# Performance work log

Hardware: AMD Instinct MI355X
Metric: run time of the kernel (lower is better)

## Reference

```python
import jax, jax.numpy as jnp
import numpy as np

DIM = 384
NH = 16
HD = DIM // NH          # 24
HID = DIM * 4           # titan/cms hidden
RD = 2 * (HD // 3 // 2) # 8 rope channels per axis (d/h/w), 3*RD == HD


def _ln(x, scale, bias):
    m = x.mean(-1, keepdims=True)
    v = ((x - m) ** 2).mean(-1, keepdims=True)
    return (x - m) * jax.lax.rsqrt(v + 1e-5) * scale + bias


def _mlp(x, w1, b1, w2, b2):
    # TitanMemory / CMS level: Linear -> GELU -> Linear (titan_layers=2)
    h = jax.nn.gelu(x @ w1 + b1, approximate=False)
    return h @ w2 + b2


def _rotate(x, pos):
    # rotate_queries_or_keys: interleaved rotary. x: [B,nh,N,d], pos: [N]
    d = x.shape[-1]
    inv_freq = 1.0 / (10000.0 ** (jnp.arange(0, d, 2, dtype=jnp.float32) / d))
    ang = pos[:, None] * inv_freq[None, :]              # [N, d/2]
    sin, cos = jnp.sin(ang), jnp.cos(ang)
    x1, x2 = x[..., 0::2], x[..., 1::2]
    y1 = x1 * cos - x2 * sin
    y2 = x1 * sin + x2 * cos
    return jnp.stack([y1, y2], axis=-1).reshape(x.shape)


def _rope3d(q, T, H, W):
    # 3D RoPE on frame tokens (action_tokens=0): time / height / width axes
    B, N, D = q.shape
    qh = q.reshape(B, N, NH, HD).transpose(0, 2, 1, 3)   # [B,nh,N,hd]
    ids = jnp.arange(T * H * W)
    tpos = (ids // (H * W)).astype(jnp.float32)
    hpos = ((ids % (H * W)) // W).astype(jnp.float32)
    wpos = (ids % W).astype(jnp.float32)
    qd = _rotate(qh[..., :RD], tpos)
    qhh = _rotate(qh[..., RD:2 * RD], hpos)
    qww = _rotate(qh[..., 2 * RD:3 * RD], wpos)
    out = jnp.concatenate([qd, qhh, qww], axis=-1)
    return out.transpose(0, 2, 1, 3).reshape(B, N, D)


def setup_inputs() -> dict:
    key = jax.random.key(0)
    ks = jax.random.split(key, 8)
    B, T, H, W = 8, 8, 16, 16
    N = T * H * W
    p = lambda k, sh: jax.random.normal(k, sh, jnp.float32) * 0.02
    return {
        "x": jax.random.normal(ks[0], (B, N, DIM), jnp.float32),
        "norm1_scale": jnp.ones((DIM,), jnp.float32),
        "norm1_bias": jnp.zeros((DIM,), jnp.float32),
        "norm2_scale": jnp.ones((DIM,), jnp.float32),
        "norm2_bias": jnp.zeros((DIM,), jnp.float32),
        "q_w": p(ks[1], (DIM, DIM)),
        # stacked Titan memories: [M_k, M_v, M_eta, M_alpha, M_memory]
        "titan_w1": p(ks[2], (5, DIM, HID)),
        "titan_b1": jnp.zeros((5, HID), jnp.float32),
        "titan_w2": p(ks[3], (5, HID, DIM)),
        "titan_b2": jnp.zeros((5, DIM), jnp.float32),
        "out_w": p(ks[4], (DIM, DIM)),
        "out_b": jnp.zeros((DIM,), jnp.float32),
        # CMS levels: [fast, medium, slow]
        "cms_w1": p(ks[5], (3, DIM, HID)),
        "cms_b1": jnp.zeros((3, HID), jnp.float32),
        "cms_w2": p(ks[6], (3, HID, DIM)),
        "cms_b2": jnp.zeros((3, DIM), jnp.float32),
        "T": T, "H": H, "W": W, "action_tokens": 0,
    }


def reference(x, norm1_scale, norm1_bias, norm2_scale, norm2_bias, q_w,
              titan_w1, titan_b1, titan_w2, titan_b2, out_w, out_b,
              cms_w1, cms_b1, cms_w2, cms_b2, T, H, W, action_tokens):
    # Phase A: self-modifying Titan (eval path: retrieval only)
    y = _ln(x, norm1_scale, norm1_bias)
    q = y @ q_w                                  # static query projection (Eq. 76)
    q = _rope3d(q, T, H, W)                      # 3D RoPE (action_tokens == 0)
    out = _mlp(q, titan_w1[4], titan_b1[4], titan_w2[4], titan_b2[4])  # M_memory(q)
    out = out @ out_w + out_b                    # out_proj
    x = x + out                                  # residual (drop_path = identity)
    # Phase B: CMS multi-frequency MLP cascade
    y = _ln(x, norm2_scale, norm2_bias)
    cms = sum(_mlp(y, cms_w1[i], cms_b1[i], cms_w2[i], cms_b2[i]) for i in range(3))
    return x + cms
```

## Files before the change

### kernel.cpp

```cpp
#include <hip/hip_runtime.h>
#include <math.h>

typedef unsigned short u16;
typedef unsigned int u32;
typedef __attribute__((ext_vector_type(8))) short short8;
typedef __attribute__((ext_vector_type(4))) float f32x4;

#define DIM 384
#define HID 1536

static __device__ __forceinline__ float bf2f(u32 b){ return __uint_as_float(b << 16); }
static __device__ __forceinline__ u16 f2bf(float f){
  u32 u = __float_as_uint(f);
  u32 r = (u + 0x7fffu + ((u >> 16) & 1u)) >> 16;
  return (u16)r;
}
static __device__ __forceinline__ float gelu_fast(float v){
  float u = v * fmaf(0.0713548162726f, v * v, 1.59576912161f);
  float e = exp2f(-1.44269504089f * u);
  return v * __builtin_amdgcn_rcpf(1.0f + e);
}
static __device__ __forceinline__ void gload_lds16(const u16* g, u16* l){
  __builtin_amdgcn_global_load_lds(
      (__attribute__((address_space(1))) void*)(void*)const_cast<u16*>(g),
      (__attribute__((address_space(3))) void*)(void*)l, 16, 0, 0);
}

__global__ __launch_bounds__(256) void ln_kernel(const float* __restrict__ x,
    const float* __restrict__ sc, const float* __restrict__ bi, u16* __restrict__ y){
  int lane = threadIdx.x & 63;
  int row = blockIdx.x * 4 + (threadIdx.x >> 6);
  const float* xr = x + (size_t)row * DIM;
  float v[6];
  float s = 0.f, sq = 0.f;
#pragma unroll
  for (int i = 0; i < 6; ++i){
    float f = xr[lane + 64*i];
    v[i] = f; s += f; sq += f*f;
  }
#pragma unroll
  for (int o = 1; o < 64; o <<= 1){ s += __shfl_xor(s, o); sq += __shfl_xor(sq, o); }
  float mean = s * (1.0f/DIM);
  float var = sq * (1.0f/DIM) - mean*mean;
  float inv = rsqrtf(var + 1e-5f);
  u16* yr = y + (size_t)row * DIM;
#pragma unroll
  for (int i = 0; i < 6; ++i){
    int c = lane + 64*i;
    yr[c] = f2bf((v[i] - mean) * inv * sc[c] + bi[c]);
  }
}

__global__ __launch_bounds__(256) void rope_kernel(u16* __restrict__ q,
    const int* __restrict__ Tp, const int* __restrict__ Hp, const int* __restrict__ Wp,
    int Mtok){
  int idx = blockIdx.x * 256 + threadIdx.x;
  int tok = idx / 192;
  if (tok >= Mtok) return;
  int p = idx - tok * 192;
  int H = *Hp, W = *Wp, T = *Tp;
  int HW = H * W;
  int Ns = T * HW;
  int n = tok % Ns;
  int head = p / 12;
  int pp = p - head * 12;
  int s = pp >> 2, f = pp & 3;
  float pos;
  if (s == 0)      pos = (float)(n / HW);
  else if (s == 1) pos = (float)((n / W) % H);
  else             pos = (float)(n % W);
  const float LOG2_10000 = 13.28771237954945f;
  float inv = exp2f(-0.25f * (float)f * LOG2_10000);
  float ang = pos * inv;
  float sn = sinf(ang), cs = cosf(ang);
  size_t base = (size_t)tok * DIM + head * 24 + s * 8 + 2 * f;
  u32 u = *(u32*)(q + base);
  float x1 = bf2f(u & 0xffffu), x2 = bf2f(u >> 16);
  float y1 = x1 * cs - x2 * sn;
  float y2 = x1 * sn + x2 * cs;
  *(u32*)(q + base) = (u32)f2bf(y1) | ((u32)f2bf(y2) << 16);
}

template<int R, int C>
__global__ __launch_bounds__(256) void transpose_kernel(
    const float* __restrict__ s0, const float* __restrict__ s1,
    const float* __restrict__ s2, const float* __restrict__ s3,
    u16* __restrict__ d0, u16* __restrict__ d1, u16* __restrict__ d2, u16* __restrict__ d3,
    int dstStride){
  const float* src = (blockIdx.z == 0) ? s0 : (blockIdx.z == 1) ? s1 : (blockIdx.z == 2) ? s2 : s3;
  u16* dst         = (blockIdx.z == 0) ? d0 : (blockIdx.z == 1) ? d1 : (blockIdx.z == 2) ? d2 : d3;
  __shared__ u16 t[32][33];
  int tx = threadIdx.x & 31, ty = threadIdx.x >> 5;
  int r0 = blockIdx.y * 32, c0 = blockIdx.x * 32;
#pragma unroll
  for (int i = 0; i < 4; ++i)
    t[ty + 8*i][tx] = f2bf(src[(size_t)(r0 + ty + 8*i) * C + c0 + tx]);
  __syncthreads();
#pragma unroll
  for (int i = 0; i < 4; ++i)
    dst[(size_t)(c0 + ty + 8*i) * dstStride + r0 + tx] = t[tx][ty + 8*i];
}

__global__ void bias3_kernel(const float* __restrict__ b, float* __restrict__ o){
  int n = threadIdx.x;
  o[n] = b[n] + b[384 + n] + b[768 + n];
}

enum { E_NONE = 0, E_BIAS = 1, E_BIAS_GELU = 2, E_RES_F32 = 3, E_ACC_F32 = 4, E_FINAL = 5 };

template<int BM, int N, int K, int EPI>
__global__ __launch_bounds__(256) void gemm_kernel(
    const u16* __restrict__ A, const u16* __restrict__ Bt,
    void* __restrict__ Cv, const float* __restrict__ bias,
    const float* __restrict__ res, float* __restrict__ accbuf){
  constexpr int BN = 128, BK = 64;
  constexpr int MT = BM / 32, NT = 4;
  constexpr int AIT = BM / 32, BIT = 4;
  __shared__ __align__(16) u16 As[BM * BK];
  __shared__ __align__(16) u16 Bs[BN * BK];
  const int tid = threadIdx.x;
  const int lane = tid & 63;
  const int wv = tid >> 6;
  const int wm = (wv >> 1) * (BM / 2);
  const int wn = (wv & 1) * 64;
  const int quad = lane >> 4;
  const int l16 = lane & 15;
  const int rsw = l16 & 7;
  const size_t m0 = (size_t)blockIdx.x * BM;
  const int n0 = blockIdx.y * BN;
  const int srow = lane >> 3;
  const int scol = ((lane & 7) ^ srow) * 8;

  f32x4 acc[MT][NT];
  const f32x4 zero = {0.f, 0.f, 0.f, 0.f};
#pragma unroll
  for (int mt = 0; mt < MT; ++mt)
#pragma unroll
    for (int nt = 0; nt < NT; ++nt) acc[mt][nt] = zero;

  for (int kt = 0; kt < K; kt += BK){
#pragma unroll
    for (int i = 0; i < AIT; ++i){
      int seg = i * 4 + wv;
      gload_lds16(A + (m0 + (size_t)(seg * 8 + srow)) * K + kt + scol, As + seg * 512);
    }
#pragma unroll
    for (int i = 0; i < BIT; ++i){
      int seg = i * 4 + wv;
      gload_lds16(Bt + (size_t)(n0 + seg * 8 + srow) * K + kt + scol, Bs + seg * 512);
    }
    __syncthreads();
#pragma unroll
    for (int kk = 0; kk < 2; ++kk){
      short8 af[MT], bfr[NT];
#pragma unroll
      for (int mt = 0; mt < MT; ++mt)
        af[mt] = *(const short8*)(As + (wm + mt*16 + l16) * BK + (((kk*4 + quad) ^ rsw) << 3));
#pragma unroll
      for (int nt = 0; nt < NT; ++nt)
        bfr[nt] = *(const short8*)(Bs + (wn + nt*16 + l16) * BK + (((kk*4 + quad) ^ rsw) << 3));
#pragma unroll
      for (int mt = 0; mt < MT; ++mt)
#pragma unroll
        for (int nt = 0; nt < NT; ++nt)
          acc[mt][nt] = __builtin_amdgcn_mfma_f32_16x16x32_bf16(af[mt], bfr[nt], acc[mt][nt], 0, 0, 0);
    }
    __syncthreads();
  }

#pragma unroll
  for (int mt = 0; mt < MT; ++mt){
#pragma unroll
    for (int nt = 0; nt < NT; ++nt){
      int ncol = n0 + wn + nt*16 + l16;
      float bv = (EPI != E_NONE) ? bias[ncol] : 0.f;
      size_t mbase = m0 + wm + mt*16 + quad*4;
#pragma unroll
      for (int r = 0; r < 4; ++r){
        size_t off = (mbase + r) * N + ncol;
        float vv = acc[mt][nt][r];
        if      (EPI == E_NONE)      ((u16*)Cv)[off] = f2bf(vv);
        else if (EPI == E_BIAS)      ((u16*)Cv)[off] = f2bf(vv + bv);
        else if (EPI == E_BIAS_GELU) ((u16*)Cv)[off] = f2bf(gelu_fast(vv + bv));
        else if (EPI == E_RES_F32)   accbuf[off] = vv + bv + res[off];
        else if (EPI == E_ACC_F32)   accbuf[off] += vv + bv;
        else            ((float*)Cv)[off] = accbuf[off] + vv + bv;
      }
    }
  }
}

template<int N, int K>
__global__ __launch_bounds__(256, 3) void gemm_up_kernel(
    const u16* __restrict__ A, const u16* __restrict__ Bt,
    u16* __restrict__ C, const float* __restrict__ bias){
  constexpr int BK = 64;
  __shared__ __align__(16) u16 As[64 * BK];
  __shared__ __align__(16) u16 Bs[256 * BK];
  const int tid = threadIdx.x;
  const int lane = tid & 63;
  const int wv = tid >> 6;
  const int wm = (wv >> 1) * 32;
  const int wn = (wv & 1) * 128;
  const int quad = lane >> 4;
  const int l16 = lane & 15;
  const int rsw = l16 & 7;
  const size_t m0 = (size_t)blockIdx.x * 64;
  const int n0 = blockIdx.y * 256;
  const int srow = lane >> 3;
  const int scol = ((lane & 7) ^ srow) * 8;

  f32x4 acc[2][8];
  const f32x4 zero = {0.f, 0.f, 0.f, 0.f};
#pragma unroll
  for (int mt = 0; mt < 2; ++mt)
#pragma unroll
    for (int nt = 0; nt < 8; ++nt) acc[mt][nt] = zero;

  for (int kt = 0; kt < K; kt += BK){
#pragma unroll
    for (int i = 0; i < 2; ++i){
      int seg = i * 4 + wv;
      gload_lds16(A + (m0 + (size_t)(seg * 8 + srow)) * K + kt + scol, As + seg * 512);
    }
#pragma unroll
    for (int i = 0; i < 8; ++i){
      int seg = i * 4 + wv;
      gload_lds16(Bt + (size_t)(n0 + seg * 8 + srow) * K + kt + scol, Bs + seg * 512);
    }
    __syncthreads();
#pragma unroll
    for (int kk = 0; kk < 2; ++kk){
      short8 af[2], bfr[8];
#pragma unroll
      for (int mt = 0; mt < 2; ++mt)
        af[mt] = *(const short8*)(As + (wm + mt*16 + l16) * BK + (((kk*4 + quad) ^ rsw) << 3));
#pragma unroll
      for (int nt = 0; nt < 8; ++nt)
        bfr[nt] = *(const short8*)(Bs + (wn + nt*16 + l16) * BK + (((kk*4 + quad) ^ rsw) << 3));
#pragma unroll
      for (int mt = 0; mt < 2; ++mt)
#pragma unroll
        for (int nt = 0; nt < 8; ++nt)
          acc[mt][nt] = __builtin_amdgcn_mfma_f32_16x16x32_bf16(af[mt], bfr[nt], acc[mt][nt], 0, 0, 0);
    }
    __syncthreads();
  }

#pragma unroll
  for (int mt = 0; mt < 2; ++mt){
#pragma unroll
    for (int nt = 0; nt < 8; ++nt){
      int ncol = n0 + wn + nt*16 + l16;
      float bv = bias[ncol];
      size_t mbase = m0 + wm + mt*16 + quad*4;
#pragma unroll
      for (int r = 0; r < 4; ++r)
        C[(mbase + r) * N + ncol] = f2bf(gelu_fast(acc[mt][nt][r] + bv));
    }
  }
}

extern "C" void kernel_launch(void* const* d_in, const int* in_sizes, int n_in,
                              void* d_out, int out_size, void* d_ws, size_t ws_size,
                              hipStream_t stream) {
  const int W11 = DIM * HID;
  const float* x   = (const float*)d_in[0];
  const float* n1s = (const float*)d_in[1];
  const float* n1b = (const float*)d_in[2];
  const float* n2s = (const float*)d_in[3];
  const float* n2b = (const float*)d_in[4];
  const float* qw  = (const float*)d_in[5];
  const float* tw1 = (const float*)d_in[6] + 4 * W11;
  const float* tb1 = (const float*)d_in[7] + 4 * HID;
  const float* tw2 = (const float*)d_in[8] + 4 * W11;
  const float* tb2 = (const float*)d_in[9] + 4 * DIM;
  const float* ow  = (const float*)d_in[10];
  const float* ob  = (const float*)d_in[11];
  const float* cw1 = (const float*)d_in[12];
  const float* cb1 = (const float*)d_in[13];
  const float* cw2 = (const float*)d_in[14];
  const float* cb2 = (const float*)d_in[15];
  const int* Tp = (const int*)d_in[16];
  const int* Hp = (const int*)d_in[17];
  const int* Wp = (const int*)d_in[18];
  const int M = in_sizes[0] / DIM;
  const bool fused = (ws_size >= 198772224u);

  char* ws = (char*)d_ws;
  u16 *y, *h, *qwT, *owT, *w1T, *w2T, *cw1T, *cw2T;
  float *x2, *cb2s = nullptr;
  u16* qb = (u16*)d_out;
  if (fused){
    y    = (u16*) (ws + 0);
    h    = (u16*) (ws + 12582912);
    x2   = (float*)(ws + 163577856);
    qwT  = (u16*) (ws + 188743680);
    owT  = (u16*) (ws + 189038592);
    w1T  = (u16*) (ws + 189333504);
    w2T  = (u16*) (ws + 190513152);
    cw1T = (u16*) (ws + 191692800);
    cw2T = (u16*) (ws + 195231744);
    cb2s = (float*)(ws + 198770688);
  } else {
    if (ws_size < 98107392u) return;
    y    = (u16*) (ws + 0);
    h    = (u16*) (ws + 12582912);
    x2   = (float*)(ws + 62914560);
    qwT  = (u16*) (ws + 88080384);
    owT  = (u16*) (ws + 88375296);
    w1T  = (u16*) (ws + 88670208);
    w2T  = (u16*) (ws + 89849856);
    cw1T = (u16*) (ws + 91029504);
    cw2T = (u16*) (ws + 94568448);
  }

  transpose_kernel<384,384><<<dim3(12,12,2),256,0,stream>>>(
      qw, ow, qw, qw, qwT, owT, qwT, qwT, 384);
  transpose_kernel<384,1536><<<dim3(48,12,4),256,0,stream>>>(
      tw1, cw1, cw1 + W11, cw1 + 2*W11, w1T, cw1T, cw1T + W11, cw1T + 2*W11, 384);
  if (fused){
    transpose_kernel<1536,384><<<dim3(12,48,1),256,0,stream>>>(
        tw2, tw2, tw2, tw2, w2T, w2T, w2T, w2T, 1536);
    transpose_kernel<1536,384><<<dim3(12,48,3),256,0,stream>>>(
        cw2, cw2 + W11, cw2 + 2*W11, cw2, cw2T, cw2T + 1536, cw2T + 3072, cw2T, 4608);
    bias3_kernel<<<1,384,0,stream>>>(cb2, cb2s);
  } else {
    transpose_kernel<1536,384><<<dim3(12,48,4),256,0,stream>>>(
        tw2, cw2, cw2 + W11, cw2 + 2*W11, w2T, cw2T, cw2T + W11, cw2T + 2*W11, 1536);
  }

  ln_kernel<<<M/4,256,0,stream>>>(x, n1s, n1b, y);
  gemm_kernel<64,384,384,E_NONE><<<dim3(M/64,3),256,0,stream>>>(y, qwT, qb, nullptr, nullptr, nullptr);
  rope_kernel<<<(M*192)/256,256,0,stream>>>(qb, Tp, Hp, Wp, M);
  gemm_up_kernel<1536,384><<<dim3(M/64,6),256,0,stream>>>(qb, w1T, h, tb1);
  gemm_kernel<64,384,1536,E_BIAS><<<dim3(M/64,3),256,0,stream>>>(h, w2T, qb, tb2, nullptr, nullptr);
  gemm_kernel<64,384,384,E_RES_F32><<<dim3(M/64,3),256,0,stream>>>(qb, owT, nullptr, ob, x, x2);
  ln_kernel<<<M/4,256,0,stream>>>(x2, n2s, n2b, y);
  if (fused){
    gemm_up_kernel<4608,384><<<dim3(M/64,18),256,0,stream>>>(y, cw1T, h, cb1);
    gemm_kernel<64,384,4608,E_FINAL><<<dim3(M/64,3),256,0,stream>>>(
        h, cw2T, d_out, cb2s, nullptr, x2);
  } else {
    for (int i = 0; i < 3; ++i){
      gemm_up_kernel<1536,384><<<dim3(M/64,6),256,0,stream>>>(y, cw1T + i*W11, h, cb1 + i*HID);
      if (i < 2)
        gemm_kernel<64,384,1536,E_ACC_F32><<<dim3(M/64,3),256,0,stream>>>(
            h, cw2T + i*W11, nullptr, cb2 + i*DIM, nullptr, x2);
      else
        gemm_kernel<64,384,1536,E_FINAL><<<dim3(M/64,3),256,0,stream>>>(
            h, cw2T + i*W11, d_out, cb2 + i*DIM, nullptr, x2);
    }
  }
}
```

Baseline: 400.1 us.

## Fuse MLP up and down projections, keeping GELU hidden chunks in LDS

```diff
diff --git a/kernel.cpp b/kernel.cpp
--- a/kernel.cpp
+++ b/kernel.cpp
@@ -17,7 +17,7 @@
 }
 static __device__ __forceinline__ float gelu_fast(float v){
   float u = v * fmaf(0.0713548162726f, v * v, 1.59576912161f);
-  float e = exp2f(-1.44269504089f * u);
+  float e = __builtin_amdgcn_exp2f(-1.44269504089f * u);
   return v * __builtin_amdgcn_rcpf(1.0f + e);
 }
 static __device__ __forceinline__ void gload_lds16(const u16* g, u16* l){
@@ -70,9 +70,9 @@
   else if (s == 1) pos = (float)((n / W) % H);
   else             pos = (float)(n % W);
   const float LOG2_10000 = 13.28771237954945f;
-  float inv = exp2f(-0.25f * (float)f * LOG2_10000);
+  float inv = __builtin_amdgcn_exp2f(-0.25f * (float)f * LOG2_10000);
   float ang = pos * inv;
-  float sn = sinf(ang), cs = cosf(ang);
+  float sn = __sinf(ang), cs = __cosf(ang);
   size_t base = (size_t)tok * DIM + head * 24 + s * 8 + 2 * f;
   u32 u = *(u32*)(q + base);
   float x1 = bf2f(u & 0xffffu), x2 = bf2f(u >> 16);
@@ -190,73 +190,139 @@
   }
 }
 
-template<int N, int K>
-__global__ __launch_bounds__(256, 3) void gemm_up_kernel(
-    const u16* __restrict__ A, const u16* __restrict__ Bt,
-    u16* __restrict__ C, const float* __restrict__ bias){
-  constexpr int BK = 64;
-  __shared__ __align__(16) u16 As[64 * BK];
-  __shared__ __align__(16) u16 Bs[256 * BK];
-  const int tid = threadIdx.x;
+template<int HIDT, int EPI>
+__global__ __launch_bounds__(512, 2) void fused_mlp_kernel(
+    const u16* __restrict__ A, const u16* __restrict__ W1t, const u16* __restrict__ W2t,
+    const float* __restrict__ b1, const float* __restrict__ b2,
+    float* __restrict__ accbuf, void* __restrict__ outp){
+  constexpr int BH = 256;
+  constexpr int NCH = HIDT / BH;
+  __shared__ __align__(16) u16 SB[(64 + BH) * 64];
+  __shared__ __align__(16) u16 Hs[4 * 64 * 64];
+  __shared__ __align__(16) u16 W2s[384 * 64];
+
+  const int tid  = threadIdx.x;
   const int lane = tid & 63;
-  const int wv = tid >> 6;
-  const int wm = (wv >> 1) * 32;
-  const int wn = (wv & 1) * 128;
+  const int wv   = tid >> 6;
   const int quad = lane >> 4;
-  const int l16 = lane & 15;
-  const int rsw = l16 & 7;
+  const int l16  = lane & 15;
   const size_t m0 = (size_t)blockIdx.x * 64;
-  const int n0 = blockIdx.y * 256;
   const int srow = lane >> 3;
   const int scol = ((lane & 7) ^ srow) * 8;
 
-  f32x4 acc[2][8];
+  const int uwm = (wv & 1) * 32;
+  const int pan = wv >> 1;
+  const int dwn = wv * 48;
+
+  f32x4 cacc[4][3];
   const f32x4 zero = {0.f, 0.f, 0.f, 0.f};
 #pragma unroll
-  for (int mt = 0; mt < 2; ++mt)
-#pragma unroll
-    for (int nt = 0; nt < 8; ++nt) acc[mt][nt] = zero;
-
-  for (int kt = 0; kt < K; kt += BK){
-#pragma unroll
-    for (int i = 0; i < 2; ++i){
-      int seg = i * 4 + wv;
-      gload_lds16(A + (m0 + (size_t)(seg * 8 + srow)) * K + kt + scol, As + seg * 512);
-    }
-#pragma unroll
-    for (int i = 0; i < 8; ++i){
-      int seg = i * 4 + wv;
-      gload_lds16(Bt + (size_t)(n0 + seg * 8 + srow) * K + kt + scol, Bs + seg * 512);
+  for (int mt = 0; mt < 4; ++mt)
+#pragma unroll
+    for (int nt = 0; nt < 3; ++nt) cacc[mt][nt] = zero;
+
+  for (int c = 0; c < NCH; ++c){
+    f32x4 hacc[2][4];
+#pragma unroll
+    for (int mt = 0; mt < 2; ++mt)
+#pragma unroll
+      for (int nt = 0; nt < 4; ++nt) hacc[mt][nt] = zero;
+
+    for (int kt = 0; kt < 384; kt += 64){
+#pragma unroll
+      for (int i = 0; i < 5; ++i){
+        int seg = i * 8 + wv;
+        const u16* src = (i == 0)
+            ? A + (m0 + (size_t)(seg * 8 + srow)) * 384 + kt + scol
+            : W1t + ((size_t)c * BH + (seg - 8) * 8 + srow) * 384 + kt + scol;
+        gload_lds16(src, SB + seg * 512);
+      }
+      __syncthreads();
+#pragma unroll
+      for (int kk = 0; kk < 2; ++kk){
+        short8 af[2], bfr[4];
+#pragma unroll
+        for (int mt = 0; mt < 2; ++mt){
+          int row = uwm + mt*16 + l16;
+          af[mt] = *(const short8*)(SB + row*64 + (((kk*4 + quad) ^ (row & 7)) << 3));
+        }
+#pragma unroll
+        for (int nt = 0; nt < 4; ++nt){
+          int row = 64 + pan*64 + nt*16 + l16;
+          bfr[nt] = *(const short8*)(SB + row*64 + (((kk*4 + quad) ^ (row & 7)) << 3));
+        }
+#pragma unroll
+        for (int mt = 0; mt < 2; ++mt)
+#pragma unroll
+          for (int nt = 0; nt < 4; ++nt)
+            hacc[mt][nt] = __builtin_amdgcn_mfma_f32_16x16x32_bf16(af[mt], bfr[nt], hacc[mt][nt], 0, 0, 0);
+      }
+      __syncthreads();
+    }
+
+#pragma unroll
+    for (int nt = 0; nt < 4; ++nt){
+      int pc = nt*16 + l16;
+      float bv = b1[c*BH + pan*64 + pc];
+      u16* hp = Hs + pan*4096;
+#pragma unroll
+      for (int mt = 0; mt < 2; ++mt){
+#pragma unroll
+        for (int r = 0; r < 4; ++r){
+          int row = uwm + mt*16 + quad*4 + r;
+          float g = gelu_fast(hacc[mt][nt][r] + bv);
+          hp[row*64 + (((pc >> 3) ^ (row & 7)) << 3) + (pc & 7)] = f2bf(g);
+        }
+      }
     }
     __syncthreads();
-#pragma unroll
-    for (int kk = 0; kk < 2; ++kk){
-      short8 af[2], bfr[8];
-#pragma unroll
-      for (int mt = 0; mt < 2; ++mt)
-        af[mt] = *(const short8*)(As + (wm + mt*16 + l16) * BK + (((kk*4 + quad) ^ rsw) << 3));
-#pragma unroll
-      for (int nt = 0; nt < 8; ++nt)
-        bfr[nt] = *(const short8*)(Bs + (wn + nt*16 + l16) * BK + (((kk*4 + quad) ^ rsw) << 3));
-#pragma unroll
-      for (int mt = 0; mt < 2; ++mt)
-#pragma unroll
-        for (int nt = 0; nt < 8; ++nt)
-          acc[mt][nt] = __builtin_amdgcn_mfma_f32_16x16x32_bf16(af[mt], bfr[nt], acc[mt][nt], 0, 0, 0);
-    }
-    __syncthreads();
-  }
-
-#pragma unroll
-  for (int mt = 0; mt < 2; ++mt){
-#pragma unroll
-    for (int nt = 0; nt < 8; ++nt){
-      int ncol = n0 + wn + nt*16 + l16;
-      float bv = bias[ncol];
-      size_t mbase = m0 + wm + mt*16 + quad*4;
-#pragma unroll
-      for (int r = 0; r < 4; ++r)
-        C[(mbase + r) * N + ncol] = f2bf(gelu_fast(acc[mt][nt][r] + bv));
+
+    for (int q = 0; q < 4; ++q){
+#pragma unroll
+      for (int i = 0; i < 6; ++i){
+        int seg = i * 8 + wv;
+        gload_lds16(W2t + (size_t)(seg * 8 + srow) * HIDT + c*BH + q*64 + scol,
+                    W2s + seg * 512);
+      }
+      __syncthreads();
+#pragma unroll
+      for (int kk = 0; kk < 2; ++kk){
+        short8 af[4], bfr[3];
+#pragma unroll
+        for (int mt = 0; mt < 4; ++mt){
+          int row = mt*16 + l16;
+          af[mt] = *(const short8*)(Hs + q*4096 + row*64 + (((kk*4 + quad) ^ (row & 7)) << 3));
+        }
+#pragma unroll
+        for (int nt = 0; nt < 3; ++nt){
+          int nrow = dwn + nt*16 + l16;
+          bfr[nt] = *(const short8*)(W2s + nrow*64 + (((kk*4 + quad) ^ (nrow & 7)) << 3));
+        }
+#pragma unroll
+        for (int mt = 0; mt < 4; ++mt)
+#pragma unroll
+          for (int nt = 0; nt < 3; ++nt)
+            cacc[mt][nt] = __builtin_amdgcn_mfma_f32_16x16x32_bf16(af[mt], bfr[nt], cacc[mt][nt], 0, 0, 0);
+      }
+      __syncthreads();
+    }
+  }
+
+#pragma unroll
+  for (int nt = 0; nt < 3; ++nt){
+    int col = dwn + nt*16 + l16;
+    float bv = b2[col];
+#pragma unroll
+    for (int mt = 0; mt < 4; ++mt){
+      size_t mbase = m0 + mt*16 + quad*4;
+#pragma unroll
+      for (int r = 0; r < 4; ++r){
+        size_t off = (mbase + r) * DIM + col;
+        float vv = cacc[mt][nt][r] + bv;
+        if      (EPI == E_BIAS)    ((u16*)outp)[off] = f2bf(vv);
+        else if (EPI == E_ACC_F32) accbuf[off] += vv;
+        else          ((float*)outp)[off] = accbuf[off] + vv;
+      }
     }
   }
 }
@@ -288,12 +354,11 @@
   const bool fused = (ws_size >= 198772224u);
 
   char* ws = (char*)d_ws;
-  u16 *y, *h, *qwT, *owT, *w1T, *w2T, *cw1T, *cw2T;
+  u16 *y, *qwT, *owT, *w1T, *w2T, *cw1T, *cw2T;
   float *x2, *cb2s = nullptr;
   u16* qb = (u16*)d_out;
   if (fused){
     y    = (u16*) (ws + 0);
-    h    = (u16*) (ws + 12582912);
     x2   = (float*)(ws + 163577856);
     qwT  = (u16*) (ws + 188743680);
     owT  = (u16*) (ws + 189038592);
@@ -305,7 +370,6 @@
   } else {
     if (ws_size < 98107392u) return;
     y    = (u16*) (ws + 0);
-    h    = (u16*) (ws + 12582912);
     x2   = (float*)(ws + 62914560);
     qwT  = (u16*) (ws + 88080384);
     owT  = (u16*) (ws + 88375296);
@@ -333,23 +397,19 @@
   ln_kernel<<<M/4,256,0,stream>>>(x, n1s, n1b, y);
   gemm_kernel<64,384,384,E_NONE><<<dim3(M/64,3),256,0,stream>>>(y, qwT, qb, nullptr, nullptr, nullptr);
   rope_kernel<<<(M*192)/256,256,0,stream>>>(qb, Tp, Hp, Wp, M);
-  gemm_up_kernel<1536,384><<<dim3(M/64,6),256,0,stream>>>(qb, w1T, h, tb1);
-  gemm_kernel<64,384,1536,E_BIAS><<<dim3(M/64,3),256,0,stream>>>(h, w2T, qb, tb2, nullptr, nullptr);
+  fused_mlp_kernel<1536,E_BIAS><<<M/64,512,0,stream>>>(qb, w1T, w2T, tb1, tb2, nullptr, qb);
   gemm_kernel<64,384,384,E_RES_F32><<<dim3(M/64,3),256,0,stream>>>(qb, owT, nullptr, ob, x, x2);
   ln_kernel<<<M/4,256,0,stream>>>(x2, n2s, n2b, y);
   if (fused){
-    gemm_up_kernel<4608,384><<<dim3(M/64,18),256,0,stream>>>(y, cw1T, h, cb1);
-    gemm_kernel<64,384,4608,E_FINAL><<<dim3(M/64,3),256,0,stream>>>(
-        h, cw2T, d_out, cb2s, nullptr, x2);
+    fused_mlp_kernel<4608,E_FINAL><<<M/64,512,0,stream>>>(y, cw1T, cw2T, cb1, cb2s, x2, d_out);
   } else {
     for (int i = 0; i < 3; ++i){
-      gemm_up_kernel<1536,384><<<dim3(M/64,6),256,0,stream>>>(y, cw1T + i*W11, h, cb1 + i*HID);
       if (i < 2)
-        gemm_kernel<64,384,1536,E_ACC_F32><<<dim3(M/64,3),256,0,stream>>>(
-            h, cw2T + i*W11, nullptr, cb2 + i*DIM, nullptr, x2);
+        fused_mlp_kernel<1536,E_ACC_F32><<<M/64,512,0,stream>>>(
+            y, cw1T + i*W11, cw2T + i*W11, cb1 + i*HID, cb2 + i*DIM, x2, nullptr);
       else
-        gemm_kernel<64,384,1536,E_FINAL><<<dim3(M/64,3),256,0,stream>>>(
-            h, cw2T + i*W11, d_out, cb2 + i*DIM, nullptr, x2);
-    }
-  }
-}
+        fused_mlp_kernel<1536,E_FINAL><<<M/64,512,0,stream>>>(
+            y, cw1T + i*W11, cw2T + i*W11, cb1 + i*HID, cb2 + i*DIM, x2, d_out);
+    }
+  }
+}
```

New measurement: 498.4 us. 24.6% more time.

## Use 512-thread 128-row GEMM tiles for MLP layers and fast intrinsics

Applied to the files above, without the earlier changes.

```diff
diff --git a/kernel.cpp b/kernel.cpp
--- a/kernel.cpp
+++ b/kernel.cpp
@@ -17,7 +17,7 @@
 }
 static __device__ __forceinline__ float gelu_fast(float v){
   float u = v * fmaf(0.0713548162726f, v * v, 1.59576912161f);
-  float e = exp2f(-1.44269504089f * u);
+  float e = __builtin_amdgcn_exp2f(-1.44269504089f * u);
   return v * __builtin_amdgcn_rcpf(1.0f + e);
 }
 static __device__ __forceinline__ void gload_lds16(const u16* g, u16* l){
@@ -70,9 +70,9 @@
   else if (s == 1) pos = (float)((n / W) % H);
   else             pos = (float)(n % W);
   const float LOG2_10000 = 13.28771237954945f;
-  float inv = exp2f(-0.25f * (float)f * LOG2_10000);
+  float inv = __builtin_amdgcn_exp2f(-0.25f * (float)f * LOG2_10000);
   float ang = pos * inv;
-  float sn = sinf(ang), cs = cosf(ang);
+  float sn = __sinf(ang), cs = __cosf(ang);
   size_t base = (size_t)tok * DIM + head * 24 + s * 8 + 2 * f;
   u32 u = *(u32*)(q + base);
   float x1 = bf2f(u & 0xffffu), x2 = bf2f(u >> 16);
@@ -106,7 +106,7 @@
   o[n] = b[n] + b[384 + n] + b[768 + n];
 }
 
-enum { E_NONE = 0, E_BIAS = 1, E_BIAS_GELU = 2, E_RES_F32 = 3, E_ACC_F32 = 4, E_FINAL = 5 };
+enum { E_NONE = 0, E_BIAS = 1, E_RES_F32 = 3, E_FINAL = 5 };
 
 template<int BM, int N, int K, int EPI>
 __global__ __launch_bounds__(256) void gemm_kernel(
@@ -181,21 +181,18 @@
         float vv = acc[mt][nt][r];
         if      (EPI == E_NONE)      ((u16*)Cv)[off] = f2bf(vv);
         else if (EPI == E_BIAS)      ((u16*)Cv)[off] = f2bf(vv + bv);
-        else if (EPI == E_BIAS_GELU) ((u16*)Cv)[off] = f2bf(gelu_fast(vv + bv));
-        else if (EPI == E_RES_F32)   accbuf[off] = vv + bv + res[off];
-        else if (EPI == E_ACC_F32)   accbuf[off] += vv + bv;
-        else            ((float*)Cv)[off] = accbuf[off] + vv + bv;
+        else          accbuf[off] = vv + bv + res[off];
       }
     }
   }
 }
 
 template<int N, int K>
-__global__ __launch_bounds__(256, 3) void gemm_up_kernel(
+__global__ __launch_bounds__(512, 4) void gemm_up2_kernel(
     const u16* __restrict__ A, const u16* __restrict__ Bt,
     u16* __restrict__ C, const float* __restrict__ bias){
   constexpr int BK = 64;
-  __shared__ __align__(16) u16 As[64 * BK];
+  __shared__ __align__(16) u16 As[128 * BK];
   __shared__ __align__(16) u16 Bs[256 * BK];
   const int tid = threadIdx.x;
   const int lane = tid & 63;
@@ -205,7 +202,7 @@
   const int quad = lane >> 4;
   const int l16 = lane & 15;
   const int rsw = l16 & 7;
-  const size_t m0 = (size_t)blockIdx.x * 64;
+  const size_t m0 = (size_t)blockIdx.x * 128;
   const int n0 = blockIdx.y * 256;
   const int srow = lane >> 3;
   const int scol = ((lane & 7) ^ srow) * 8;
@@ -220,12 +217,12 @@
   for (int kt = 0; kt < K; kt += BK){
 #pragma unroll
     for (int i = 0; i < 2; ++i){
-      int seg = i * 4 + wv;
+      int seg = i * 8 + wv;
       gload_lds16(A + (m0 + (size_t)(seg * 8 + srow)) * K + kt + scol, As + seg * 512);
     }
 #pragma unroll
-    for (int i = 0; i < 8; ++i){
-      int seg = i * 4 + wv;
+    for (int i = 0; i < 4; ++i){
+      int seg = i * 8 + wv;
       gload_lds16(Bt + (size_t)(n0 + seg * 8 + srow) * K + kt + scol, Bs + seg * 512);
     }
     __syncthreads();
@@ -257,6 +254,78 @@
 #pragma unroll
       for (int r = 0; r < 4; ++r)
         C[(mbase + r) * N + ncol] = f2bf(gelu_fast(acc[mt][nt][r] + bv));
+    }
+  }
+}
+
+template<int N, int K, int EPI>
+__global__ __launch_bounds__(512, 4) void gemm2_kernel(
+    const u16* __restrict__ A, const u16* __restrict__ Bt,
+    void* __restrict__ Cv, const float* __restrict__ bias,
+    const float* __restrict__ accbuf){
+  constexpr int BK = 64;
+  __shared__ __align__(16) u16 As[128 * BK];
+  __shared__ __align__(16) u16 Bs[128 * BK];
+  const int tid = threadIdx.x;
+  const int lane = tid & 63;
+  const int wv = tid >> 6;
+  const int wm = (wv >> 1) * 32;
+  const int wn = (wv & 1) * 64;
+  const int quad = lane >> 4;
+  const int l16 = lane & 15;
+  const int rsw = l16 & 7;
+  const size_t m0 = (size_t)blockIdx.x * 128;
+  const int n0 = blockIdx.y * 128;
+  const int srow = lane >> 3;
+  const int scol = ((lane & 7) ^ srow) * 8;
+
+  f32x4 acc[2][4];
+  const f32x4 zero = {0.f, 0.f, 0.f, 0.f};
+#pragma unroll
+  for (int mt = 0; mt < 2; ++mt)
+#pragma unroll
+    for (int nt = 0; nt < 4; ++nt) acc[mt][nt] = zero;
+
+  for (int kt = 0; kt < K; kt += BK){
+#pragma unroll
+    for (int i = 0; i < 2; ++i){
+      int seg = i * 8 + wv;
+      gload_lds16(A + (m0 + (size_t)(seg * 8 + srow)) * K + kt + scol, As + seg * 512);
+      gload_lds16(Bt + (size_t)(n0 + seg * 8 + srow) * K + kt + scol, Bs + seg * 512);
+    }
+    __syncthreads();
+#pragma unroll
+    for (int kk = 0; kk < 2; ++kk){
+      short8 af[2], bfr[4];
+#pragma unroll
+      for (int mt = 0; mt < 2; ++mt)
+        af[mt] = *(const short8*)(As + (wm + mt*16 + l16) * BK + (((kk*4 + quad) ^ rsw) << 3));
+#pragma unroll
+      for (int nt = 0; nt < 4; ++nt)
+        bfr[nt] = *(const short8*)(Bs + (wn + nt*16 + l16) * BK + (((kk*4 + quad) ^ rsw) << 3));
+#pragma unroll
+      for (int mt = 0; mt < 2; ++mt)
+#pragma unroll
+        for (int nt = 0; nt < 4; ++nt)
+          acc[mt][nt] = __builtin_amdgcn_mfma_f32_16x16x32_bf16(af[mt], bfr[nt], acc[mt][nt], 0, 0, 0);
+    }
+    __syncthreads();
+  }
+
+#pragma unroll
+  for (int mt = 0; mt < 2; ++mt){
+#pragma unroll
+    for (int nt = 0; nt < 4; ++nt){
+      int ncol = n0 + wn + nt*16 + l16;
+      float bv = bias[ncol];
+      size_t mbase = m0 + wm + mt*16 + quad*4;
+#pragma unroll
+      for (int r = 0; r < 4; ++r){
+        size_t off = (mbase + r) * N + ncol;
+        float vv = acc[mt][nt][r] + bv;
+        if (EPI == E_BIAS) ((u16*)Cv)[off] = f2bf(vv);
+        else  ((float*)Cv)[off] = accbuf[off] + vv;
+      }
     }
   }
 }
@@ -285,71 +354,38 @@
   const int* Hp = (const int*)d_in[17];
   const int* Wp = (const int*)d_in[18];
   const int M = in_sizes[0] / DIM;
-  const bool fused = (ws_size >= 198772224u);
 
   char* ws = (char*)d_ws;
-  u16 *y, *h, *qwT, *owT, *w1T, *w2T, *cw1T, *cw2T;
-  float *x2, *cb2s = nullptr;
-  u16* qb = (u16*)d_out;
-  if (fused){
-    y    = (u16*) (ws + 0);
-    h    = (u16*) (ws + 12582912);
-    x2   = (float*)(ws + 163577856);
-    qwT  = (u16*) (ws + 188743680);
-    owT  = (u16*) (ws + 189038592);
-    w1T  = (u16*) (ws + 189333504);
-    w2T  = (u16*) (ws + 190513152);
-    cw1T = (u16*) (ws + 191692800);
-    cw2T = (u16*) (ws + 195231744);
-    cb2s = (float*)(ws + 198770688);
-  } else {
-    if (ws_size < 98107392u) return;
-    y    = (u16*) (ws + 0);
-    h    = (u16*) (ws + 12582912);
-    x2   = (float*)(ws + 62914560);
-    qwT  = (u16*) (ws + 88080384);
-    owT  = (u16*) (ws + 88375296);
-    w1T  = (u16*) (ws + 88670208);
-    w2T  = (u16*) (ws + 89849856);
-    cw1T = (u16*) (ws + 91029504);
-    cw2T = (u16*) (ws + 94568448);
-  }
+  if (ws_size < 198772224u) return;
+  u16*  y    = (u16*) (ws + 0);
+  u16*  h    = (u16*) (ws + 12582912);
+  float* x2  = (float*)(ws + 163577856);
+  u16*  qwT  = (u16*) (ws + 188743680);
+  u16*  owT  = (u16*) (ws + 189038592);
+  u16*  w1T  = (u16*) (ws + 189333504);
+  u16*  w2T  = (u16*) (ws + 190513152);
+  u16*  cw1T = (u16*) (ws + 191692800);
+  u16*  cw2T = (u16*) (ws + 195231744);
+  float* cb2s = (float*)(ws + 198770688);
+  u16*  qb   = (u16*)d_out;
 
   transpose_kernel<384,384><<<dim3(12,12,2),256,0,stream>>>(
       qw, ow, qw, qw, qwT, owT, qwT, qwT, 384);
   transpose_kernel<384,1536><<<dim3(48,12,4),256,0,stream>>>(
       tw1, cw1, cw1 + W11, cw1 + 2*W11, w1T, cw1T, cw1T + W11, cw1T + 2*W11, 384);
-  if (fused){
-    transpose_kernel<1536,384><<<dim3(12,48,1),256,0,stream>>>(
-        tw2, tw2, tw2, tw2, w2T, w2T, w2T, w2T, 1536);
-    transpose_kernel<1536,384><<<dim3(12,48,3),256,0,stream>>>(
-        cw2, cw2 + W11, cw2 + 2*W11, cw2, cw2T, cw2T + 1536, cw2T + 3072, cw2T, 4608);
-    bias3_kernel<<<1,384,0,stream>>>(cb2, cb2s);
-  } else {
-    transpose_kernel<1536,384><<<dim3(12,48,4),256,0,stream>>>(
-        tw2, cw2, cw2 + W11, cw2 + 2*W11, w2T, cw2T, cw2T + W11, cw2T + 2*W11, 1536);
-  }
+  transpose_kernel<1536,384><<<dim3(12,48,1),256,0,stream>>>(
+      tw2, tw2, tw2, tw2, w2T, w2T, w2T, w2T, 1536);
+  transpose_kernel<1536,384><<<dim3(12,48,3),256,0,stream>>>(
+      cw2, cw2 + W11, cw2 + 2*W11, cw2, cw2T, cw2T + 1536, cw2T + 3072, cw2T, 4608);
+  bias3_kernel<<<1,384,0,stream>>>(cb2, cb2s);
 
   ln_kernel<<<M/4,256,0,stream>>>(x, n1s, n1b, y);
   gemm_kernel<64,384,384,E_NONE><<<dim3(M/64,3),256,0,stream>>>(y, qwT, qb, nullptr, nullptr, nullptr);
   rope_kernel<<<(M*192)/256,256,0,stream>>>(qb, Tp, Hp, Wp, M);
-  gemm_up_kernel<1536,384><<<dim3(M/64,6),256,0,stream>>>(qb, w1T, h, tb1);
-  gemm_kernel<64,384,1536,E_BIAS><<<dim3(M/64,3),256,0,stream>>>(h, w2T, qb, tb2, nullptr, nullptr);
+  gemm_up2_kernel<1536,384><<<dim3(M/128,6),512,0,stream>>>(qb, w1T, h, tb1);
+  gemm2_kernel<384,1536,E_BIAS><<<dim3(M/128,3),512,0,stream>>>(h, w2T, qb, tb2, nullptr);
   gemm_kernel<64,384,384,E_RES_F32><<<dim3(M/64,3),256,0,stream>>>(qb, owT, nullptr, ob, x, x2);
   ln_kernel<<<M/4,256,0,stream>>>(x2, n2s, n2b, y);
-  if (fused){
-    gemm_up_kernel<4608,384><<<dim3(M/64,18),256,0,stream>>>(y, cw1T, h, cb1);
-    gemm_kernel<64,384,4608,E_FINAL><<<dim3(M/64,3),256,0,stream>>>(
-        h, cw2T, d_out, cb2s, nullptr, x2);
-  } else {
-    for (int i = 0; i < 3; ++i){
-      gemm_up_kernel<1536,384><<<dim3(M/64,6),256,0,stream>>>(y, cw1T + i*W11, h, cb1 + i*HID);
-      if (i < 2)
-        gemm_kernel<64,384,1536,E_ACC_F32><<<dim3(M/64,3),256,0,stream>>>(
-            h, cw2T + i*W11, nullptr, cb2 + i*DIM, nullptr, x2);
-      else
-        gemm_kernel<64,384,1536,E_FINAL><<<dim3(M/64,3),256,0,stream>>>(
-            h, cw2T + i*W11, d_out, cb2 + i*DIM, nullptr, x2);
-    }
-  }
-}
+  gemm_up2_kernel<4608,384><<<dim3(M/128,18),512,0,stream>>>(y, cw1T, h, cb1);
+  gemm2_kernel<384,4608,E_FINAL><<<dim3(M/128,3),512,0,stream>>>(h, cw2T, d_out, cb2s, x2);
+}
```

After: 394.1 us (median of 2 runs). About the same (-1.5%).
